# Performance work log

Measured on AMD Instinct MI355X. Metric: run time of the kernel, lower is better.

Reference implementation:

```python
import jax, jax.numpy as jnp
import numpy as np

HIDDEN = 512


def _lstm(x, kernel, rec, bias):
    # x: [B,T,D]; Keras gate order i,f,c(g),o
    xz = jnp.einsum('btd,dk->btk', x, kernel) + bias  # [B,T,4H]
    B = x.shape[0]
    init = (jnp.zeros((B, HIDDEN), x.dtype), jnp.zeros((B, HIDDEN), x.dtype))

    def step(carry, z_t):
        h, c = carry
        z = z_t + h @ rec
        i, f, g, o = jnp.split(z, 4, axis=-1)
        c = jax.nn.sigmoid(f) * c + jax.nn.sigmoid(i) * jnp.tanh(g)
        h = jax.nn.sigmoid(o) * jnp.tanh(c)
        return (h, c), h

    _, hs = jax.lax.scan(step, init, jnp.swapaxes(xz, 0, 1))
    return jnp.swapaxes(hs, 0, 1)  # [B,T,H]


def _bilstm(x, kf, rf, bf, kb, rb, bb):
    fwd = _lstm(x, kf, rf, bf)
    bwd = _lstm(x[:, ::-1], kb, rb, bb)[:, ::-1]
    return jnp.concatenate([fwd, bwd], axis=-1)  # [B,T,2H]


def _crf_nll(logits, tags, seq_lens, trans):
    # logits [B,T,N], tags [B,T] int, seq_lens [B] int, trans [N,N]
    B, T, N = logits.shape
    t_idx = jnp.arange(T)
    mask = (t_idx[None, :] < seq_lens[:, None])  # [B,T] bool
    maskf = mask.astype(logits.dtype)

    # gold sequence score: unary + pairwise transitions
    unary = jnp.take_along_axis(logits, tags[..., None], axis=-1)[..., 0]  # [B,T]
    unary_score = jnp.sum(unary * maskf, axis=-1)
    pair_maskf = maskf[:, 1:]  # pair (t-1,t) valid iff t < len
    binary = trans[tags[:, :-1], tags[:, 1:]]  # [B,T-1]
    binary_score = jnp.sum(binary * pair_maskf, axis=-1)

    # log-partition via forward algorithm (masked scan)
    alpha0 = logits[:, 0]  # [B,N]

    def step(alpha, inp):
        logit_t, valid = inp
        new = jax.nn.logsumexp(alpha[:, :, None] + trans[None], axis=1) + logit_t
        return jnp.where(valid[:, None], new, alpha), None

    xs = (jnp.swapaxes(logits[:, 1:], 0, 1), jnp.swapaxes(mask[:, 1:], 0, 1))
    alpha, _ = jax.lax.scan(step, alpha0, xs)
    log_z = jax.nn.logsumexp(alpha, axis=-1)  # [B]
    return -(unary_score + binary_score - log_z)


def setup_inputs() -> dict:
    key = jax.random.key(0)
    ks = jax.random.split(key, 12)
    B, T, D, H, N = 32, 256, 768, HIDDEN, 25
    s_in = 1.0 / np.sqrt(D)
    s_rec = 1.0 / np.sqrt(H)
    return {
        'embeddings': jax.random.normal(ks[0], (B, T, D), jnp.float32),
        'targets': jax.random.randint(ks[1], (B, T), 0, N, jnp.int32),
        'seq_lens': jax.random.randint(ks[2], (B,), 1, T + 1, jnp.int32),
        'k_fwd': jax.random.normal(ks[3], (D, 4 * H), jnp.float32) * s_in,
        'r_fwd': jax.random.normal(ks[4], (H, 4 * H), jnp.float32) * s_rec,
        'b_fwd': jnp.zeros((4 * H,), jnp.float32),
        'k_bwd': jax.random.normal(ks[5], (D, 4 * H), jnp.float32) * s_in,
        'r_bwd': jax.random.normal(ks[6], (H, 4 * H), jnp.float32) * s_rec,
        'b_bwd': jnp.zeros((4 * H,), jnp.float32),
        'dense_w': jax.random.normal(ks[7], (2 * H, N), jnp.float32) / np.sqrt(2 * H),
        'dense_b': jnp.zeros((N,), jnp.float32),
        'transitions': jax.random.uniform(ks[8], (N, N), jnp.float32),
    }


def reference(embeddings, targets, seq_lens, k_fwd, r_fwd, b_fwd,
              k_bwd, r_bwd, b_bwd, dense_w, dense_b, transitions):
    seq_lens = jnp.clip(seq_lens, 1, embeddings.shape[1])
    h = _bilstm(embeddings, k_fwd, r_fwd, b_fwd, k_bwd, r_bwd, b_bwd)
    logits = jax.nn.selu(jnp.einsum('bth,hn->btn', h, dense_w) + dense_b)
    nll = _crf_nll(logits, targets, seq_lens, transitions)  # [B]
    loss = jnp.mean(nll)
    return loss, logits
```

## Files before the change

kernel.cpp:

```cpp
#include <hip/hip_runtime.h>
#include <hip/hip_bf16.h>
#include <math.h>

#define HID 512
#define GATES 2048
#define BT 8192
#define TT 256
#define BB 32
#define DIN 768
#define NTAG 25
#define UPB 4
#define NBLK 128
#define FSTR 4
#define EREP 8
#define ESTR 16

typedef _Float16 half2v __attribute__((ext_vector_type(2)));
typedef _Float16 half8  __attribute__((ext_vector_type(8)));
typedef float    f32x4  __attribute__((ext_vector_type(4)));

__device__ __forceinline__ half2v pack2h(float a, float b) {
  return __builtin_bit_cast(half2v, __builtin_amdgcn_cvt_pkrtz(a, b));
}

__device__ __forceinline__ float sigf(float x) { return 1.f / (1.f + __expf(-x)); }

__global__ __launch_bounds__(256) void transpose_k(
    const float* __restrict__ Kf, const float* __restrict__ Kb,
    unsigned short* __restrict__ KTf, unsigned short* __restrict__ KTb)
{
  const int dir = blockIdx.z;
  const float* __restrict__ K = dir ? Kb : Kf;
  unsigned short* __restrict__ KT = dir ? KTb : KTf;
  const int k0 = blockIdx.x * 64;
  const int n0 = blockIdx.y * 64;
  __shared__ float tile[64][65];
  const int tid = threadIdx.x;
  #pragma unroll
  for (int p = 0; p < 4; ++p) {
    const int idx = p * 256 + tid;
    const int kr = idx >> 4, c4 = (idx & 15) * 4;
    const float4 v = *(const float4*)(K + (size_t)(k0 + kr) * GATES + n0 + c4);
    tile[kr][c4 + 0] = v.x; tile[kr][c4 + 1] = v.y;
    tile[kr][c4 + 2] = v.z; tile[kr][c4 + 3] = v.w;
  }
  __syncthreads();
  #pragma unroll
  for (int p = 0; p < 2; ++p) {
    const int idx = p * 256 + tid;
    const int nr = idx >> 3, s = (idx & 7) * 8;
    half8 hv;
    #pragma unroll
    for (int x = 0; x < 8; ++x) hv[x] = (_Float16)tile[s + x][nr];
    *(half8*)(KT + (size_t)(n0 + nr) * DIN + k0 + s) = hv;
  }
}

__global__ __launch_bounds__(256) void gemm_xz(
    const float* __restrict__ emb,
    const unsigned short* __restrict__ KTf, const unsigned short* __restrict__ KTb,
    const float* __restrict__ bf, const float* __restrict__ bb,
    float* __restrict__ xzf, float* __restrict__ xzb)
{
  const int dir = blockIdx.z;
  const unsigned short* __restrict__ KT = dir ? KTb : KTf;
  const float* __restrict__ bias = dir ? bb : bf;
  float* __restrict__ C = dir ? xzb : xzf;
  const int n0 = blockIdx.x * 128;
  const int m0 = blockIdx.y * 128;

  __shared__ __align__(16) char A_lds[128 * 64 * 2];
  __shared__ __align__(16) char B_lds[128 * 64 * 2];

  const int tid = threadIdx.x;
  const int lane = tid & 63, wid = tid >> 6;
  const int wm = wid >> 1, wn = wid & 1;
  const int lm = lane & 15, lk = lane >> 4;

  f32x4 acc[4][4];
  #pragma unroll
  for (int i = 0; i < 4; ++i)
    #pragma unroll
    for (int j = 0; j < 4; ++j) acc[i][j] = (f32x4){0.f, 0.f, 0.f, 0.f};

  for (int kt = 0; kt < DIN / 64; ++kt) {
    const int k0 = kt * 64;
    __syncthreads();
    #pragma unroll
    for (int p = 0; p < 4; ++p) {
      const int id = p * 256 + tid;
      const int r = id >> 3, s = id & 7;
      const float* src = emb + (size_t)(m0 + r) * DIN + k0 + s * 8;
      const float4 v0 = *(const float4*)(src);
      const float4 v1 = *(const float4*)(src + 4);
      half8 hv;
      hv[0] = (_Float16)v0.x; hv[1] = (_Float16)v0.y;
      hv[2] = (_Float16)v0.z; hv[3] = (_Float16)v0.w;
      hv[4] = (_Float16)v1.x; hv[5] = (_Float16)v1.y;
      hv[6] = (_Float16)v1.z; hv[7] = (_Float16)v1.w;
      *(half8*)(A_lds + r * 128 + ((s ^ (r & 7)) << 4)) = hv;
    }
    #pragma unroll
    for (int p = 0; p < 4; ++p) {
      const int id = p * 256 + tid;
      const int r = id >> 3, s = id & 7;
      const uint4 v = *(const uint4*)(KT + (size_t)(n0 + r) * DIN + k0 + s * 8);
      *(uint4*)(B_lds + r * 128 + ((s ^ (r & 7)) << 4)) = v;
    }
    __syncthreads();

    #pragma unroll
    for (int kh = 0; kh < 2; ++kh) {
      half8 a[4], b[4];
      #pragma unroll
      for (int mt = 0; mt < 4; ++mt) {
        const int rloc = wm * 64 + mt * 16 + lm;
        const int kslot = kh * 4 + lk;
        a[mt] = *(const half8*)(A_lds + rloc * 128 + ((kslot ^ (rloc & 7)) << 4));
      }
      #pragma unroll
      for (int nt = 0; nt < 4; ++nt) {
        const int nloc = wn * 64 + nt * 16 + lm;
        const int kslot = kh * 4 + lk;
        b[nt] = *(const half8*)(B_lds + nloc * 128 + ((kslot ^ (nloc & 7)) << 4));
      }
      #pragma unroll
      for (int mt = 0; mt < 4; ++mt)
        #pragma unroll
        for (int nt = 0; nt < 4; ++nt)
          acc[mt][nt] = __builtin_amdgcn_mfma_f32_16x16x32_f16(a[mt], b[nt], acc[mt][nt], 0, 0, 0);
    }
  }

  #pragma unroll
  for (int nt = 0; nt < 4; ++nt) {
    const int col = n0 + wn * 64 + nt * 16 + lm;
    const float bs = bias[col];
    #pragma unroll
    for (int mt = 0; mt < 4; ++mt) {
      const int rowb = m0 + wm * 64 + mt * 16 + lk * 4;
      const f32x4 v = acc[mt][nt];
      #pragma unroll
      for (int g = 0; g < 4; ++g)
        C[(size_t)(rowb + g) * GATES + col] = v[g] + bs;
    }
  }
}

__global__ __launch_bounds__(256, 1) void lstm_persist(
    const float* __restrict__ xzf, const float* __restrict__ xzb,
    const float* __restrict__ Rf, const float* __restrict__ Rb,
    unsigned int* __restrict__ hGf, unsigned int* __restrict__ hGb,
    int* __restrict__ flg,
    int* __restrict__ ep)
{
  const int bid = blockIdx.x;
  const int dir = bid & 1;
  const int blk = bid >> 1;
  const int u0 = blk * UPB;
  const int tid = threadIdx.x;
  const int c = tid & 15;
  const int j = (c & 3) * HID + u0 + (c >> 2);
  const int lane = tid & 63, w = tid >> 6;
  const int lm = lane & 15, lk = lane >> 4;

  const float* __restrict__ R  = dir ? Rb : Rf;
  const float* __restrict__ xz = dir ? xzb : xzf;
  unsigned int* __restrict__ hGd = dir ? hGb : hGf;
  int* __restrict__ flgd = flg + (size_t)dir * TT * NBLK * FSTR;
  int* __restrict__ epd  = ep  + (size_t)dir * TT * EREP * ESTR;

  __shared__ uint4 hs4[BB * 65];
  __shared__ float redm[4][BB][18];
  __shared__ float zbuf[BB][20];

  half8 Rbf[4];
  #pragma unroll
  for (int kti = 0; kti < 4; ++kti) {
    const int kb = (w * 4 + kti) * 32 + lk * 8;
    half8 hv;
    #pragma unroll
    for (int x = 0; x < 8; ++x) hv[x] = (_Float16)R[(size_t)(kb + x) * GATES + j];
    Rbf[kti] = hv;
  }

  float cst = 0.f;
  const int b_o = tid & 31, u_o = tid >> 5;
  const int fb0 = tid >> 4, fb1 = (tid >> 4) + 16;
  const bool leader = (blk == 0);

  for (int s = 0; s < TT; ++s) {
    const int t = dir ? (TT - 1 - s) : s;

    const float x0 = xz[((size_t)fb0 * TT + t) * GATES + j];
    const float x1 = xz[((size_t)fb1 * TT + t) * GATES + j];

    if (s > 0) {
      const int tprev = dir ? t + 1 : t - 1;
      if (leader) {
        if (tid < NBLK) {
          while (!__hip_atomic_load(&flgd[((s - 1) * NBLK + tid) * FSTR],
                                    __ATOMIC_RELAXED, __HIP_MEMORY_SCOPE_AGENT))
            __builtin_amdgcn_s_sleep(1);
        }
        __syncthreads();
        if (tid < EREP)
          __hip_atomic_store(&epd[((s - 1) * EREP + tid) * ESTR], 1,
                             __ATOMIC_RELAXED, __HIP_MEMORY_SCOPE_AGENT);
      } else {
        if (tid == 0) {
          while (!__hip_atomic_load(&epd[((s - 1) * EREP + (blk & 7)) * ESTR],
                                    __ATOMIC_RELAXED, __HIP_MEMORY_SCOPE_AGENT))
            __builtin_amdgcn_s_sleep(1);
        }
        __syncthreads();
      }
      const uint4* hsrc = (const uint4*)(hGd + (size_t)tprev * BB * 256);
      #pragma unroll
      for (int it = 0; it < 8; ++it) {
        const int g4 = tid + it * 256;
        const uint4 v = hsrc[g4];
        hs4[(g4 >> 6) * 65 + (g4 & 63)] = v;
      }
    } else {
      const uint4 zz = make_uint4(0u, 0u, 0u, 0u);
      #pragma unroll
      for (int it = 0; it < 9; ++it) {
        const int idx = tid + it * 256;
        if (idx < BB * 65) hs4[idx] = zz;
      }
    }
    __syncthreads();

    f32x4 acc0 = (f32x4){0.f, 0.f, 0.f, 0.f};
    f32x4 acc1 = (f32x4){0.f, 0.f, 0.f, 0.f};
    #pragma unroll
    for (int kti = 0; kti < 4; ++kti) {
      const int k4 = (w * 4 + kti) * 4 + lk;
      const half8 a0 = *(const half8*)&hs4[(lm) * 65 + k4];
      const half8 a1 = *(const half8*)&hs4[(16 + lm) * 65 + k4];
      acc0 = __builtin_amdgcn_mfma_f32_16x16x32_f16(a0, Rbf[kti], acc0, 0, 0, 0);
      acc1 = __builtin_amdgcn_mfma_f32_16x16x32_f16(a1, Rbf[kti], acc1, 0, 0, 0);
    }
    #pragma unroll
    for (int g = 0; g < 4; ++g) {
      redm[w][lk * 4 + g][lm] = acc0[g];
      redm[w][16 + lk * 4 + g][lm] = acc1[g];
    }
    __syncthreads();

    {
      const float za = redm[0][fb0][c] + redm[1][fb0][c] + redm[2][fb0][c] + redm[3][fb0][c] + x0;
      const float zb2 = redm[0][fb1][c] + redm[1][fb1][c] + redm[2][fb1][c] + redm[3][fb1][c] + x1;
      zbuf[fb0][c] = za;
      zbuf[fb1][c] = zb2;
    }
    __syncthreads();

    if (tid < 128) {
      const float zi = zbuf[b_o][u_o * 4 + 0];
      const float zf = zbuf[b_o][u_o * 4 + 1];
      const float zg = zbuf[b_o][u_o * 4 + 2];
      const float zo = zbuf[b_o][u_o * 4 + 3];
      cst = sigf(zf) * cst + sigf(zi) * tanhf(zg);
      const float h = sigf(zo) * tanhf(cst);
      const float hp2 = __shfl_xor(h, 32);
      if ((tid & 32) == 0) {
        const half2v p = pack2h(h, hp2);
        __hip_atomic_store(&hGd[((size_t)t * BB + b_o) * 256 + blk * 2 + (u_o >> 1)],
                           __builtin_bit_cast(unsigned int, p),
                           __ATOMIC_RELAXED, __HIP_MEMORY_SCOPE_AGENT);
      }
    }
    __syncthreads();
    if (tid == 0)
      __hip_atomic_store(&flgd[(s * NBLK + blk) * FSTR], 1, __ATOMIC_RELAXED,
                         __HIP_MEMORY_SCOPE_AGENT);
  }
}

__global__ __launch_bounds__(256) void dense_selu(
    const unsigned int* __restrict__ hGf, const unsigned int* __restrict__ hGb,
    const float* __restrict__ W, const float* __restrict__ bias,
    float* __restrict__ out)
{
  const int bt = blockIdx.x;
  const int b = bt >> 8, t = bt & 255;
  __shared__ float h[1024];
  __shared__ float part[8][33];
  const int tid = threadIdx.x;
  {
    const unsigned int wf = hGf[((size_t)t * BB + b) * 256 + tid];
    const unsigned int wb = hGb[((size_t)t * BB + b) * 256 + tid];
    const half2v f = __builtin_bit_cast(half2v, wf);
    const half2v g = __builtin_bit_cast(half2v, wb);
    h[2 * tid]       = (float)f.x;
    h[2 * tid + 1]   = (float)f.y;
    h[512 + 2 * tid]     = (float)g.x;
    h[512 + 2 * tid + 1] = (float)g.y;
  }
  __syncthreads();
  const int n = tid & 31, s8 = tid >> 5;
  if (n < NTAG) {
    float acc = 0.f;
    const int k0 = s8 * 128;
    #pragma unroll 4
    for (int k = k0; k < k0 + 128; ++k) acc = fmaf(h[k], W[(size_t)k * NTAG + n], acc);
    part[s8][n] = acc;
  }
  __syncthreads();
  if (tid < NTAG) {
    float v = 0.f;
    #pragma unroll
    for (int q = 0; q < 8; ++q) v += part[q][tid];
    v += bias[tid];
    const float scale = 1.0507009873554805f, alf = 1.6732632423543772f;
    v = v > 0.f ? scale * v : scale * alf * (__expf(v) - 1.f);
    out[(size_t)bt * NTAG + tid] = v;
  }
}

__global__ __launch_bounds__(64) void crf_kernel(
    const float* __restrict__ logits,
    const int* __restrict__ tags, const int* __restrict__ lens,
    const float* __restrict__ trans, float* __restrict__ nll)
{
  const int b = blockIdx.x;
  const int tid = threadIdx.x;
  __shared__ float tr[NTAG * NTAG];
  __shared__ float al[NTAG];
  __shared__ float red[2];
  for (int i = tid; i < NTAG * NTAG; i += 64) tr[i] = trans[i];
  __syncthreads();

  int len = lens[b];
  len = len < 1 ? 1 : (len > TT ? TT : len);
  const size_t base = (size_t)b * TT;

  float us = 0.f, bs = 0.f;
  for (int t = tid; t < TT; t += 64) {
    if (t < len) us += logits[(base + t) * NTAG + tags[base + t]];
    if (t >= 1 && t < len) bs += tr[tags[base + t - 1] * NTAG + tags[base + t]];
  }
  #pragma unroll
  for (int off = 32; off > 0; off >>= 1) {
    us += __shfl_down(us, off);
    bs += __shfl_down(bs, off);
  }
  if (tid == 0) { red[0] = us; red[1] = bs; }

  if (tid < NTAG) al[tid] = logits[base * NTAG + tid];
  __syncthreads();

  for (int t = 1; t < len; ++t) {
    float nv = 0.f;
    if (tid < NTAG) {
      float m = -3.4e38f;
      #pragma unroll
      for (int i = 0; i < NTAG; ++i) m = fmaxf(m, al[i] + tr[i * NTAG + tid]);
      float ss = 0.f;
      #pragma unroll
      for (int i = 0; i < NTAG; ++i) ss += __expf(al[i] + tr[i * NTAG + tid] - m);
      nv = m + __logf(ss) + logits[(base + t) * NTAG + tid];
    }
    __syncthreads();
    if (tid < NTAG) al[tid] = nv;
    __syncthreads();
  }

  if (tid == 0) {
    float m = -3.4e38f;
    for (int i = 0; i < NTAG; ++i) m = fmaxf(m, al[i]);
    float ss = 0.f;
    for (int i = 0; i < NTAG; ++i) ss += __expf(al[i] - m);
    const float logz = m + __logf(ss);
    nll[b] = -(red[0] + red[1] - logz);
  }
}

__global__ __launch_bounds__(64) void finalize(const float* __restrict__ nll, float* __restrict__ out) {
  float v = (threadIdx.x < BB) ? nll[threadIdx.x] : 0.f;
  #pragma unroll
  for (int off = 32; off > 0; off >>= 1) v += __shfl_down(v, off);
  if (threadIdx.x == 0) out[0] = v * (1.f / BB);
}

extern "C" void kernel_launch(void* const* d_in, const int* in_sizes, int n_in,
                              void* d_out, int out_size, void* d_ws, size_t ws_size,
                              hipStream_t stream) {
  const float* emb  = (const float*)d_in[0];
  const int* tags   = (const int*)d_in[1];
  const int* lens   = (const int*)d_in[2];
  const float* kf   = (const float*)d_in[3];
  const float* rf   = (const float*)d_in[4];
  const float* bf   = (const float*)d_in[5];
  const float* kb   = (const float*)d_in[6];
  const float* rb   = (const float*)d_in[7];
  const float* bb   = (const float*)d_in[8];
  const float* dw   = (const float*)d_in[9];
  const float* db   = (const float*)d_in[10];
  const float* trans= (const float*)d_in[11];
  float* out = (float*)d_out;

  float* ws  = (float*)d_ws;
  float* xzf = ws;
  float* xzb = xzf + (size_t)BT * GATES;
  unsigned int* hGf = (unsigned int*)(xzb + (size_t)BT * GATES);
  unsigned int* hGb = hGf + (size_t)TT * BB * 256;
  unsigned short* KTf = (unsigned short*)(hGb + (size_t)TT * BB * 256);
  unsigned short* KTb = KTf + (size_t)GATES * DIN;
  float* nll = (float*)(KTb + (size_t)GATES * DIN);
  int*   flg = (int*)(nll + 64);
  int*   ep  = flg + 2 * TT * NBLK * FSTR;

  (void)hipMemsetAsync(flg, 0,
                       (size_t)(2 * TT * NBLK * FSTR + 2 * TT * EREP * ESTR) * 4,
                       stream);

  transpose_k<<<dim3(DIN / 64, GATES / 64, 2), 256, 0, stream>>>(kf, kb, KTf, KTb);
  gemm_xz<<<dim3(GATES / 128, BT / 128, 2), 256, 0, stream>>>(emb, KTf, KTb, bf, bb, xzf, xzb);
  lstm_persist<<<2 * NBLK, 256, 0, stream>>>(xzf, xzb, rf, rb, hGf, hGb, flg, ep);
  dense_selu<<<8192, 256, 0, stream>>>(hGf, hGb, dw, db, out + 1);
  crf_kernel<<<32, 64, 0, stream>>>(out + 1, tags, lens, trans, nll);
  finalize<<<1, 64, 0, stream>>>(nll, out);
}
```

Before: 982.1 us.

## Pre-convert inputs to fp16, use direct global-to-LDS loads, MFMA dense layer

Embeddings are converted once to fp16 in a pre-swizzled layout, and the K transpose writes the same swizzled layout. This lets gemm_xz fill LDS with global_load_lds instead of loading, converting and storing through registers. The dense+SELU stage becomes a tiled MFMA GEMM over 128-row blocks with fp16 weights, replacing 8192 scalar-FMA blocks. The cost is extra conversion kernels and workspace, and the dense layer now runs in fp16 inputs with a padded N dimension.

```diff
diff --git a/kernel.cpp b/kernel.cpp
--- a/kernel.cpp
+++ b/kernel.cpp
@@ -25,6 +25,33 @@
 
 __device__ __forceinline__ float sigf(float x) { return 1.f / (1.f + __expf(-x)); }
 
+__device__ __forceinline__ void gld_lds16(const void* g, void* l) {
+  __builtin_amdgcn_global_load_lds(
+      (const __attribute__((address_space(1))) unsigned int*)g,
+      (__attribute__((address_space(3))) unsigned int*)l, 16, 0, 0);
+}
+
+__global__ __launch_bounds__(256) void convert_emb(
+    const float* __restrict__ emb, unsigned short* __restrict__ emb16)
+{
+  const int m = blockIdx.x * 8 + (threadIdx.x >> 5);
+  const int c0 = threadIdx.x & 31;
+  #pragma unroll
+  for (int p = 0; p < 3; ++p) {
+    const int c = c0 + p * 32;
+    const int kb = c >> 3, s = c & 7;
+    const float* src = emb + (size_t)m * DIN + c * 8;
+    const float4 v0 = *(const float4*)src;
+    const float4 v1 = *(const float4*)(src + 4);
+    half8 hv;
+    hv[0] = (_Float16)v0.x; hv[1] = (_Float16)v0.y;
+    hv[2] = (_Float16)v0.z; hv[3] = (_Float16)v0.w;
+    hv[4] = (_Float16)v1.x; hv[5] = (_Float16)v1.y;
+    hv[6] = (_Float16)v1.z; hv[7] = (_Float16)v1.w;
+    *(half8*)(emb16 + (size_t)m * DIN + kb * 64 + (s ^ (m & 7)) * 8) = hv;
+  }
+}
+
 __global__ __launch_bounds__(256) void transpose_k(
     const float* __restrict__ Kf, const float* __restrict__ Kb,
     unsigned short* __restrict__ KTf, unsigned short* __restrict__ KTb)
@@ -48,16 +75,26 @@
   #pragma unroll
   for (int p = 0; p < 2; ++p) {
     const int idx = p * 256 + tid;
-    const int nr = idx >> 3, s = (idx & 7) * 8;
+    const int nr = idx >> 3, s = idx & 7;
     half8 hv;
     #pragma unroll
-    for (int x = 0; x < 8; ++x) hv[x] = (_Float16)tile[s + x][nr];
-    *(half8*)(KT + (size_t)(n0 + nr) * DIN + k0 + s) = hv;
+    for (int x = 0; x < 8; ++x) hv[x] = (_Float16)tile[s * 8 + x][nr];
+    *(half8*)(KT + (size_t)(n0 + nr) * DIN + k0 + (s ^ (nr & 7)) * 8) = hv;
+  }
+}
+
+__global__ __launch_bounds__(256) void prep_w(
+    const float* __restrict__ W, unsigned short* __restrict__ WT16)
+{
+  for (int id = threadIdx.x; id < 32 * 1024; id += 256) {
+    const int n = id >> 10, k = id & 1023;
+    const float v = (n < NTAG) ? W[(size_t)k * NTAG + n] : 0.f;
+    ((_Float16*)WT16)[id] = (_Float16)v;
   }
 }
 
 __global__ __launch_bounds__(256) void gemm_xz(
-    const float* __restrict__ emb,
+    const unsigned short* __restrict__ emb16,
     const unsigned short* __restrict__ KTf, const unsigned short* __restrict__ KTb,
     const float* __restrict__ bf, const float* __restrict__ bb,
     float* __restrict__ xzf, float* __restrict__ xzb)
@@ -84,28 +121,15 @@
     for (int j = 0; j < 4; ++j) acc[i][j] = (f32x4){0.f, 0.f, 0.f, 0.f};
 
   for (int kt = 0; kt < DIN / 64; ++kt) {
-    const int k0 = kt * 64;
-    __syncthreads();
-    #pragma unroll
-    for (int p = 0; p < 4; ++p) {
-      const int id = p * 256 + tid;
-      const int r = id >> 3, s = id & 7;
-      const float* src = emb + (size_t)(m0 + r) * DIN + k0 + s * 8;
-      const float4 v0 = *(const float4*)(src);
-      const float4 v1 = *(const float4*)(src + 4);
-      half8 hv;
-      hv[0] = (_Float16)v0.x; hv[1] = (_Float16)v0.y;
-      hv[2] = (_Float16)v0.z; hv[3] = (_Float16)v0.w;
-      hv[4] = (_Float16)v1.x; hv[5] = (_Float16)v1.y;
-      hv[6] = (_Float16)v1.z; hv[7] = (_Float16)v1.w;
-      *(half8*)(A_lds + r * 128 + ((s ^ (r & 7)) << 4)) = hv;
-    }
-    #pragma unroll
-    for (int p = 0; p < 4; ++p) {
-      const int id = p * 256 + tid;
-      const int r = id >> 3, s = id & 7;
-      const uint4 v = *(const uint4*)(KT + (size_t)(n0 + r) * DIN + k0 + s * 8);
-      *(uint4*)(B_lds + r * 128 + ((s ^ (r & 7)) << 4)) = v;
+    __syncthreads();
+    #pragma unroll
+    for (int i = 0; i < 4; ++i) {
+      const int g = wid * 256 + i * 64 + lane;
+      const int r = g >> 3, s = g & 7;
+      gld_lds16(emb16 + (size_t)(m0 + r) * DIN + (kt * 8 + s) * 8,
+                A_lds + (size_t)(wid * 256 + i * 64) * 16);
+      gld_lds16(KT + (size_t)(n0 + r) * DIN + (kt * 8 + s) * 8,
+                B_lds + (size_t)(wid * 256 + i * 64) * 16);
     }
     __syncthreads();
 
@@ -281,42 +305,86 @@
 
 __global__ __launch_bounds__(256) void dense_selu(
     const unsigned int* __restrict__ hGf, const unsigned int* __restrict__ hGb,
-    const float* __restrict__ W, const float* __restrict__ bias,
+    const unsigned short* __restrict__ WT16, const float* __restrict__ bias,
     float* __restrict__ out)
 {
-  const int bt = blockIdx.x;
-  const int b = bt >> 8, t = bt & 255;
-  __shared__ float h[1024];
-  __shared__ float part[8][33];
+  const int q0 = blockIdx.x * 128;
+  __shared__ __align__(16) char A_lds[128 * 64 * 2];
+  __shared__ __align__(16) char B_lds[32 * 64 * 2];
+
   const int tid = threadIdx.x;
-  {
-    const unsigned int wf = hGf[((size_t)t * BB + b) * 256 + tid];
-    const unsigned int wb = hGb[((size_t)t * BB + b) * 256 + tid];
-    const half2v f = __builtin_bit_cast(half2v, wf);
-    const half2v g = __builtin_bit_cast(half2v, wb);
-    h[2 * tid]       = (float)f.x;
-    h[2 * tid + 1]   = (float)f.y;
-    h[512 + 2 * tid]     = (float)g.x;
-    h[512 + 2 * tid + 1] = (float)g.y;
-  }
-  __syncthreads();
-  const int n = tid & 31, s8 = tid >> 5;
-  if (n < NTAG) {
-    float acc = 0.f;
-    const int k0 = s8 * 128;
-    #pragma unroll 4
-    for (int k = k0; k < k0 + 128; ++k) acc = fmaf(h[k], W[(size_t)k * NTAG + n], acc);
-    part[s8][n] = acc;
-  }
-  __syncthreads();
-  if (tid < NTAG) {
-    float v = 0.f;
-    #pragma unroll
-    for (int q = 0; q < 8; ++q) v += part[q][tid];
-    v += bias[tid];
-    const float scale = 1.0507009873554805f, alf = 1.6732632423543772f;
-    v = v > 0.f ? scale * v : scale * alf * (__expf(v) - 1.f);
-    out[(size_t)bt * NTAG + tid] = v;
+  const int lane = tid & 63, w = tid >> 6;
+  const int lm = lane & 15, lk = lane >> 4;
+
+  f32x4 acc[2][2];
+  #pragma unroll
+  for (int i = 0; i < 2; ++i)
+    #pragma unroll
+    for (int jj = 0; jj < 2; ++jj) acc[i][jj] = (f32x4){0.f, 0.f, 0.f, 0.f};
+
+  for (int kt = 0; kt < 16; ++kt) {
+    const int k0 = kt * 64;
+    __syncthreads();
+    #pragma unroll
+    for (int p = 0; p < 4; ++p) {
+      const int id = p * 256 + tid;
+      const int r = id >> 3, s = id & 7;
+      const int k = k0 + s * 8;
+      const unsigned int* src = (k < 512)
+          ? hGf + (size_t)(q0 + r) * 256 + (k >> 1)
+          : hGb + (size_t)(q0 + r) * 256 + ((k - 512) >> 1);
+      const uint4 v = *(const uint4*)src;
+      *(uint4*)(A_lds + r * 128 + ((s ^ (r & 7)) << 4)) = v;
+    }
+    {
+      const int r = tid >> 3, s = tid & 7;
+      const uint4 v = *(const uint4*)(WT16 + (size_t)r * 1024 + k0 + s * 8);
+      *(uint4*)(B_lds + r * 128 + ((s ^ (r & 7)) << 4)) = v;
+    }
+    __syncthreads();
+
+    #pragma unroll
+    for (int kh = 0; kh < 2; ++kh) {
+      const int kslot = kh * 4 + lk;
+      half8 a[2], b[2];
+      #pragma unroll
+      for (int mt = 0; mt < 2; ++mt) {
+        const int rloc = w * 32 + mt * 16 + lm;
+        a[mt] = *(const half8*)(A_lds + rloc * 128 + ((kslot ^ (rloc & 7)) << 4));
+      }
+      #pragma unroll
+      for (int nt = 0; nt < 2; ++nt) {
+        const int nloc = nt * 16 + lm;
+        b[nt] = *(const half8*)(B_lds + nloc * 128 + ((kslot ^ (nloc & 7)) << 4));
+      }
+      #pragma unroll
+      for (int mt = 0; mt < 2; ++mt)
+        #pragma unroll
+        for (int nt = 0; nt < 2; ++nt)
+          acc[mt][nt] = __builtin_amdgcn_mfma_f32_16x16x32_f16(a[mt], b[nt], acc[mt][nt], 0, 0, 0);
+    }
+  }
+
+  const float scale = 1.0507009873554805f, alf = 1.6732632423543772f;
+  #pragma unroll
+  for (int nt = 0; nt < 2; ++nt) {
+    const int col = nt * 16 + lm;
+    if (col < NTAG) {
+      const float bs = bias[col];
+      #pragma unroll
+      for (int mt = 0; mt < 2; ++mt) {
+        const int rowb = q0 + w * 32 + mt * 16 + lk * 4;
+        const f32x4 vv = acc[mt][nt];
+        #pragma unroll
+        for (int g = 0; g < 4; ++g) {
+          const int q = rowb + g;
+          const int bt = (q & 31) * 256 + (q >> 5);
+          float v = vv[g] + bs;
+          v = v > 0.f ? scale * v : scale * alf * (__expf(v) - 1.f);
+          out[(size_t)bt * NTAG + col] = v;
+        }
+      }
+    }
   }
 }
 
@@ -407,9 +475,11 @@
   float* xzb = xzf + (size_t)BT * GATES;
   unsigned int* hGf = (unsigned int*)(xzb + (size_t)BT * GATES);
   unsigned int* hGb = hGf + (size_t)TT * BB * 256;
-  unsigned short* KTf = (unsigned short*)(hGb + (size_t)TT * BB * 256);
+  unsigned short* emb16 = (unsigned short*)(hGb + (size_t)TT * BB * 256);
+  unsigned short* KTf = emb16 + (size_t)BT * DIN;
   unsigned short* KTb = KTf + (size_t)GATES * DIN;
-  float* nll = (float*)(KTb + (size_t)GATES * DIN);
+  unsigned short* WT16 = KTb + (size_t)GATES * DIN;
+  float* nll = (float*)(WT16 + 32 * 1024);
   int*   flg = (int*)(nll + 64);
   int*   ep  = flg + 2 * TT * NBLK * FSTR;
 
@@ -417,10 +487,12 @@
                        (size_t)(2 * TT * NBLK * FSTR + 2 * TT * EREP * ESTR) * 4,
                        stream);
 
+  convert_emb<<<BT / 8, 256, 0, stream>>>(emb, emb16);
   transpose_k<<<dim3(DIN / 64, GATES / 64, 2), 256, 0, stream>>>(kf, kb, KTf, KTb);
-  gemm_xz<<<dim3(GATES / 128, BT / 128, 2), 256, 0, stream>>>(emb, KTf, KTb, bf, bb, xzf, xzb);
+  prep_w<<<1, 256, 0, stream>>>(dw, WT16);
+  gemm_xz<<<dim3(GATES / 128, BT / 128, 2), 256, 0, stream>>>(emb16, KTf, KTb, bf, bb, xzf, xzb);
   lstm_persist<<<2 * NBLK, 256, 0, stream>>>(xzf, xzb, rf, rb, hGf, hGb, flg, ep);
-  dense_selu<<<8192, 256, 0, stream>>>(hGf, hGb, dw, db, out + 1);
+  dense_selu<<<BT / 128, 256, 0, stream>>>(hGf, hGb, WT16, db, out + 1);
   crf_kernel<<<32, 64, 0, stream>>>(out + 1, tags, lens, trans, nll);
   finalize<<<1, 64, 0, stream>>>(nll, out);
 }
```

Result: no change. 973.0 us (-0.9%).
